# Kernel optimization log

Measured on AMD Instinct MI355X. Metric: run time of the kernel, lower is better.

The kernel has to match this reference:

```python
import jax, jax.numpy as jnp
import numpy as np

N = 50000      # nodes
E = 800000     # edges (before self-loops)
F_IN = 128     # input node features
H = 5          # attention heads
C = 32         # per-head channels (hidden_channels // 5)
HC = H * C     # 160 = hidden_channels
G = 64         # graphs in batch


def setup_inputs() -> dict:
    key = jax.random.key(0)
    ks = jax.random.split(key, 20)
    p = lambda k, shape: jax.random.normal(k, shape, dtype=jnp.float32) * 0.1
    return {
        "x": jax.random.normal(ks[0], (N, F_IN), dtype=jnp.float32),
        "edge_index": jax.random.randint(ks[1], (2, E), 0, N),
        "edge_attr": jax.random.normal(ks[2], (E, 1), dtype=jnp.float32),
        "batch": jnp.sort(jax.random.randint(ks[3], (N,), 0, G)),
        # conv1 params (GATConv: lin, lin_edge, att_src, att_dst, att_edge, bias)
        "w1": p(ks[4], (F_IN, HC)), "we1": p(ks[5], (1, HC)),
        "as1": p(ks[6], (H, C)), "ad1": p(ks[7], (H, C)), "ae1": p(ks[8], (H, C)),
        "b1": jnp.zeros((HC,), jnp.float32),
        # conv2 params
        "w2": p(ks[9], (HC, HC)), "we2": p(ks[10], (1, HC)),
        "as2": p(ks[11], (H, C)), "ad2": p(ks[12], (H, C)), "ae2": p(ks[13], (H, C)),
        "b2": jnp.zeros((HC,), jnp.float32),
        # LayerNorms + merge MLP
        "ln1_g": jnp.ones((HC,), jnp.float32), "ln1_b": jnp.zeros((HC,), jnp.float32),
        "ln2_g": jnp.ones((HC,), jnp.float32), "ln2_b": jnp.zeros((HC,), jnp.float32),
        "mw": p(ks[14], (HC, HC)), "mb": jnp.zeros((HC,), jnp.float32),
    }


def _layernorm(x, g, b, eps=1e-5):
    m = x.mean(-1, keepdims=True)
    v = ((x - m) ** 2).mean(-1, keepdims=True)
    return (x - m) / jnp.sqrt(v + eps) * g + b


def _gat_layer(x, edge_index, edge_attr, w, we, a_s, a_d, a_e, b):
    """PyG GATConv with edge_dim, add_self_loops=True, fill_value='mean'."""
    src, dst = edge_index[0], edge_index[1]
    # self-loop edge_attr = mean of incoming edge attrs (scatter-mean onto dst)
    cnt = jax.ops.segment_sum(jnp.ones((E,), x.dtype), dst, num_segments=N)
    ea_mean = jax.ops.segment_sum(edge_attr, dst, num_segments=N) / jnp.maximum(cnt, 1.0)[:, None]
    loop = jnp.arange(N)
    src_f = jnp.concatenate([src, loop])
    dst_f = jnp.concatenate([dst, loop])
    ea_f = jnp.concatenate([edge_attr, ea_mean], axis=0)  # [E+N, 1]

    h = (x @ w).reshape(N, H, C)                           # [N,H,C]
    al_src = jnp.einsum('nhc,hc->nh', h, a_s)              # [N,H]
    al_dst = jnp.einsum('nhc,hc->nh', h, a_d)
    eh = (ea_f @ we).reshape(-1, H, C)                     # [E+N,H,C]
    al_e = jnp.einsum('ehc,hc->eh', eh, a_e)

    alpha = jax.nn.leaky_relu(al_src[src_f] + al_dst[dst_f] + al_e, 0.2)  # [E+N,H]
    amax = jax.ops.segment_max(alpha, dst_f, num_segments=N)
    ex = jnp.exp(alpha - amax[dst_f])
    den = jax.ops.segment_sum(ex, dst_f, num_segments=N)
    alpha = ex / den[dst_f]                                # segment softmax over dst

    out = jax.ops.segment_sum(h[src_f] * alpha[..., None], dst_f, num_segments=N)
    return out.reshape(N, HC) + b, alpha


def reference(x, edge_index, edge_attr, batch,
              w1, we1, as1, ad1, ae1, b1,
              w2, we2, as2, ad2, ae2, b2,
              ln1_g, ln1_b, ln2_g, ln2_b, mw, mb):
    x1, a1 = _gat_layer(x, edge_index, edge_attr, w1, we1, as1, ad1, ae1, b1)
    x1 = jax.nn.leaky_relu(x1, 0.01)
    x1 = _layernorm(x1, ln1_g, ln1_b)          # dropout = identity in eval
    x2, a2 = _gat_layer(x1, edge_index, edge_attr, w2, we2, as2, ad2, ae2, b2)
    x2 = jax.nn.leaky_relu(x2, 0.01)
    x2 = _layernorm(x2, ln2_g, ln2_b)
    x3 = jax.nn.leaky_relu(x2 @ mw + mb, 0.01)
    gcnt = jax.ops.segment_sum(jnp.ones((N,), x3.dtype), batch, num_segments=G)
    pooled = jax.ops.segment_sum(x3, batch, num_segments=G) / jnp.maximum(gcnt, 1.0)[:, None]
    return x3, pooled, a1, a2
```

## Files before the change

### kernel.cpp

```cpp
#include <hip/hip_runtime.h>
#include <hip/hip_fp16.h>
#include <math.h>

#define NN 50000
#define EE 800000
#define FIN 128
#define NH 5
#define HC 160
#define NG 64
#define CH 128
#define NB 160
#define EPB 5000
#define NW 12500
#define ALS8 8
#define LOG2E 1.4426950408889634f

typedef _Float16 f16x8 __attribute__((ext_vector_type(8)));
typedef _Float16 f16x4 __attribute__((ext_vector_type(4)));
typedef float f32x4 __attribute__((ext_vector_type(4)));

__device__ __forceinline__ float lrelu(float x, float s) { return x >= 0.f ? x : s * x; }

__device__ __forceinline__ float4 h8_to_f4(uint2 u) {
    __half2 a = *reinterpret_cast<__half2*>(&u.x);
    __half2 b = *reinterpret_cast<__half2*>(&u.y);
    float2 fa = __half22float2(a), fb = __half22float2(b);
    return make_float4(fa.x, fa.y, fb.x, fb.y);
}

__global__ void prep_kernel(const int* __restrict__ batch, float* psum, int* gcnt,
                            const float* we1, const float* ae1,
                            const float* we2, const float* ae2, float* s_out) {
    int i = blockIdx.x * 256 + threadIdx.x;
    if (i < NG * HC) psum[i] = 0.f;
    if (i < NG) {
        int lo = 0, hi = NN;
        while (lo < hi) { int m = (lo + hi) >> 1; if (batch[m] < i) lo = m + 1; else hi = m; }
        int s = lo;
        lo = 0; hi = NN;
        int g1 = i + 1;
        while (lo < hi) { int m = (lo + hi) >> 1; if (batch[m] < g1) lo = m + 1; else hi = m; }
        gcnt[i] = lo - s;
    }
    if (i < 10) {
        const float* we = (i < 5) ? we1 : we2;
        const float* ae = (i < 5) ? ae1 : ae2;
        int h = i % 5;
        float s = 0.f;
        for (int c = 0; c < 32; c++) s += we[h * 32 + c] * ae[h * 32 + c];
        s_out[i] = s * LOG2E;
    }
}

__global__ void prepw_kernel(const float* __restrict__ w1, const float* __restrict__ w2,
                             const float* __restrict__ mw,
                             __half* wt1, __half* wt2, __half* wt3) {
    int i = blockIdx.x * 256 + threadIdx.x;
    if (i < 160 * 128) {
        int c = i >> 7, k = i & 127;
        wt1[i] = __float2half(w1[k * HC + c]);
    }
    if (i < 160 * 160) {
        int c = i / 160, k = i - c * 160;
        wt2[i] = __float2half(w2[k * HC + c]);
        wt3[i] = __float2half(mw[k * HC + c]);
    }
}

__global__ __launch_bounds__(256) void hist_kernel(const int* __restrict__ ei,
                                                   unsigned* __restrict__ hist_g) {
    __shared__ unsigned lh[NW];
    int b = blockIdx.x, tid = threadIdx.x;
    for (int w = tid; w < NW; w += 256) lh[w] = 0;
    __syncthreads();
    const int* dstp = ei + EE + b * EPB;
    for (int i = tid; i < EPB; i += 256) {
        int d = dstp[i];
        atomicAdd(&lh[d >> 2], 1u << ((d & 3) * 8));
    }
    __syncthreads();
    unsigned* outp = hist_g + (size_t)b * NW;
    for (int w = tid; w < NW; w += 256) outp[w] = lh[w];
}

__global__ void sscan_kernel(const unsigned* __restrict__ hist_g,
                             unsigned short* __restrict__ base_g, int* __restrict__ deg) {
    int w = blockIdx.x * 256 + threadIdx.x;
    if (w >= NW) return;
    unsigned r0 = 0, r1 = 0, r2 = 0, r3 = 0;
    for (int b = 0; b < NB; b++) {
        unsigned x = hist_g[(size_t)b * NW + w];
        uint2 st;
        st.x = r0 | (r1 << 16);
        st.y = r2 | (r3 << 16);
        *reinterpret_cast<uint2*>(&base_g[(size_t)b * NN + 4 * w]) = st;
        r0 += x & 0xffu; r1 += (x >> 8) & 0xffu; r2 += (x >> 16) & 0xffu; r3 += (x >> 24) & 0xffu;
    }
    uint4 dv; dv.x = r0; dv.y = r1; dv.z = r2; dv.w = r3;
    *reinterpret_cast<uint4*>(&deg[4 * w]) = dv;
}

__global__ void scan1_kernel(const int* __restrict__ deg, int* bsum) {
    __shared__ int ws[4];
    int tid = threadIdx.x, lane = tid & 63, wid = tid >> 6;
    int i = blockIdx.x * 256 + tid;
    int v = (i < NN) ? deg[i] : 0;
    for (int o = 32; o >= 1; o >>= 1) v += __shfl_down(v, o, 64);
    if (lane == 0) ws[wid] = v;
    __syncthreads();
    if (tid == 0) bsum[blockIdx.x] = ws[0] + ws[1] + ws[2] + ws[3];
}

__global__ void scan2_kernel(int* bsum, int* boff) {
    __shared__ int ws[4];
    int tid = threadIdx.x, lane = tid & 63, wid = tid >> 6;
    int v = (tid < 196) ? bsum[tid] : 0;
    int x = v;
    for (int o = 1; o < 64; o <<= 1) {
        int t = __shfl_up(x, o, 64);
        if (lane >= o) x += t;
    }
    if (lane == 63) ws[wid] = x;
    __syncthreads();
    if (tid == 0) {
        int acc = 0;
        for (int w = 0; w < 4; w++) { int t = ws[w]; ws[w] = acc; acc += t; }
    }
    __syncthreads();
    if (tid < 196) boff[tid] = x + ws[wid] - v;
}

__global__ void scan3_kernel(const int* __restrict__ deg, const int* __restrict__ boff,
                             int* off) {
    __shared__ int ws[4];
    int tid = threadIdx.x, lane = tid & 63, wid = tid >> 6;
    int i = blockIdx.x * 256 + tid;
    int v = (i < NN) ? deg[i] : 0;
    int x = v;
    for (int o = 1; o < 64; o <<= 1) {
        int t = __shfl_up(x, o, 64);
        if (lane >= o) x += t;
    }
    if (lane == 63) ws[wid] = x;
    __syncthreads();
    if (tid == 0) {
        int acc = 0;
        for (int w = 0; w < 4; w++) { int t = ws[w]; ws[w] = acc; acc += t; }
    }
    __syncthreads();
    int incl = x + ws[wid] + boff[blockIdx.x];
    if (i < NN) off[i + 1] = incl;
    if (i == 0) off[0] = 0;
}

__global__ __launch_bounds__(256) void scatter_kernel(const int* __restrict__ ei,
                                                      const float* __restrict__ ea,
                                                      const unsigned short* __restrict__ base_g,
                                                      const int* __restrict__ soff,
                                                      uint4* __restrict__ erec) {
    __shared__ unsigned lc[NW];
    int b = blockIdx.x, tid = threadIdx.x;
    for (int w = tid; w < NW; w += 256) lc[w] = 0;
    __syncthreads();
    int e0 = b * EPB;
    const unsigned short* brow = base_g + (size_t)b * NN;
    for (int i = tid; i < EPB; i += 256) {
        int e = e0 + i;
        int d = ei[EE + e];
        int sh = (d & 3) * 8;
        unsigned old = atomicAdd(&lc[d >> 2], 1u << sh);
        int r = (int)((old >> sh) & 0xffu);
        int pos = soff[d] + (int)brow[d] + r;
        uint4 rec;
        rec.x = (unsigned)ei[e];
        rec.y = (unsigned)e;
        rec.z = __float_as_uint(ea[e]);
        rec.w = 0;
        erec[pos] = rec;
    }
}

template <int K, typename AT>
__global__ __launch_bounds__(128, 3) void gemm_kernel(const AT* __restrict__ A,
                                                      const __half* __restrict__ Wt,
                                                      const float* __restrict__ a_s,
                                                      const float* __restrict__ a_d,
                                                      __half* __restrict__ out,
                                                      float* __restrict__ al_s,
                                                      float* __restrict__ al_d) {
    __shared__ __align__(16) _Float16 Alds[32 * 40];
    __shared__ __align__(16) _Float16 Bt[160 * 40];
    __shared__ __align__(16) _Float16 Clds[2 * 32 * 88];
    __shared__ float asld[160], adld[160];
    const int tid = threadIdx.x;
    const int w = tid >> 6, l = tid & 63;
    const int lr = l & 15, lq = l >> 4;
    const int base = blockIdx.x * 32;

    for (int i = tid; i < 160; i += 128) { asld[i] = a_s[i]; adld[i] = a_d[i]; }

    f32x4 acc[2][5];
#pragma unroll
    for (int mt = 0; mt < 2; mt++)
#pragma unroll
        for (int t = 0; t < 5; t++) acc[mt][t] = (f32x4){0.f, 0.f, 0.f, 0.f};

    for (int k0 = 0; k0 < K; k0 += 32) {
        __syncthreads();
        if constexpr (sizeof(AT) == 4) {
            for (int f = tid; f < 256; f += 128) {
                int row = f >> 3, q = f & 7;
                float4 av = make_float4(0.f, 0.f, 0.f, 0.f);
                if (base + row < NN)
                    av = *reinterpret_cast<const float4*>(&A[(size_t)(base + row) * K + k0 + q * 4]);
                f16x4 hv = {(_Float16)av.x, (_Float16)av.y, (_Float16)av.z, (_Float16)av.w};
                *reinterpret_cast<f16x4*>(&Alds[row * 40 + q * 4]) = hv;
            }
        } else {
            int row = tid >> 2, q = tid & 3;
            uint4 v = make_uint4(0, 0, 0, 0);
            if (base + row < NN)
                v = *reinterpret_cast<const uint4*>(&A[(size_t)(base + row) * K + k0 + q * 8]);
            *reinterpret_cast<uint4*>(&Alds[row * 40 + q * 8]) = v;
        }
        for (int f = tid; f < 640; f += 128) {
            int c = f >> 2, q = f & 3;
            uint4 v = *reinterpret_cast<const uint4*>(&Wt[(size_t)c * K + k0 + q * 8]);
            *reinterpret_cast<uint4*>(&Bt[c * 40 + q * 8]) = v;
        }
        __syncthreads();
        const f16x8 a0 = *reinterpret_cast<const f16x8*>(&Alds[lr * 40 + lq * 8]);
        const f16x8 a1 = *reinterpret_cast<const f16x8*>(&Alds[(16 + lr) * 40 + lq * 8]);
#pragma unroll
        for (int t = 0; t < 5; t++) {
            const f16x8 b = *reinterpret_cast<const f16x8*>(
                &Bt[((w * 5 + t) * 16 + lr) * 40 + lq * 8]);
            acc[0][t] = __builtin_amdgcn_mfma_f32_16x16x32_f16(a0, b, acc[0][t], 0, 0, 0);
            acc[1][t] = __builtin_amdgcn_mfma_f32_16x16x32_f16(a1, b, acc[1][t], 0, 0, 0);
        }
    }
    _Float16* Cw = Clds + w * (32 * 88);
#pragma unroll
    for (int mt = 0; mt < 2; mt++)
#pragma unroll
        for (int t = 0; t < 5; t++)
#pragma unroll
            for (int j = 0; j < 4; j++)
                Cw[(mt * 16 + lq * 4 + j) * 88 + t * 16 + lr] = (_Float16)acc[mt][t][j];
    __syncthreads();
    for (int i = l; i < 320; i += 64) {
        int row = i / 10, q = i - row * 10;
        if (base + row < NN) {
            uint4 v = *reinterpret_cast<const uint4*>(&Cw[row * 88 + q * 8]);
            *reinterpret_cast<uint4*>(&out[(size_t)(base + row) * HC + w * 80 + q * 8]) = v;
        }
    }
    for (int f = tid; f < 320; f += 128) {
        int row = f / 10, rem = f - row * 10;
        int h = rem >> 1, sd = rem & 1;
        if (base + row < NN) {
            const float* av = (sd ? adld : asld) + h * 32;
            float s = 0.f;
#pragma unroll
            for (int c = 0; c < 32; c++) {
                int col = h * 32 + c;
                int wv = col >= 80;
                s += (float)Clds[wv * (32 * 88) + row * 88 + (col - 80 * wv)] * av[c];
            }
            s *= LOG2E;
            if (sd) al_d[(size_t)(base + row) * NH + h] = s;
            else    al_s[(size_t)(base + row) * ALS8 + h] = s;
        }
    }
}

__global__ __launch_bounds__(256, 8) void aggregate_kernel(
    const int* __restrict__ soff, const uint4* __restrict__ erec,
    const __half* __restrict__ hfeat, const float* __restrict__ als,
    const float* __restrict__ al_d, const float* __restrict__ s_e,
    const float* __restrict__ bias, const float* __restrict__ g_ln,
    const float* __restrict__ b_ln,
    float* __restrict__ alpha_out, __half* __restrict__ x_out) {
    const int wave = threadIdx.x >> 6;
    const int lane = threadIdx.x & 63;
    const int n = blockIdx.x * 4 + wave;
    __shared__ float w_sh_all[4][CH * NH];
    __shared__ int ioff_all[4][CH];
    float* w_sh = w_sh_all[wave];
    int* ioff_sh = ioff_all[wave];

    const int s0 = soff[n];
    const int deg = soff[n + 1] - s0;
    const int items = deg + 1;

    float adr[NH], ser[NH];
#pragma unroll
    for (int h = 0; h < NH; h++) { adr[h] = al_d[n * NH + h]; ser[h] = s_e[h]; }

    const int c0 = 4 * lane;
    const int hd = lane >> 3;
    float4 acc = make_float4(0.f, 0.f, 0.f, 0.f);

    if (items <= CH) {
        float rw[2][NH];
        float lm[NH];
#pragma unroll
        for (int h = 0; h < NH; h++) lm[h] = -3.0e38f;
        float eas = 0.f;
        int myy[2];
#pragma unroll
        for (int t = 0; t < 2; t++) {
            int i = lane + 64 * t;
            if (i < deg) {
                uint4 rec = erec[s0 + i];
                int src = (int)rec.x;
                float eav = __uint_as_float(rec.z);
                ioff_sh[i] = src * (HC * 2);
                myy[t] = (int)rec.y;
                eas += eav;
                const float* ap = als + (size_t)src * ALS8;
                float4 a4 = *reinterpret_cast<const float4*>(ap);
                float a5 = ap[4];
                float asv[5] = {a4.x, a4.y, a4.z, a4.w, a5};
#pragma unroll
                for (int h = 0; h < NH; h++) {
                    float r = lrelu(asv[h] + adr[h] + eav * ser[h], 0.2f);
                    rw[t][h] = r;
                    lm[h] = fmaxf(lm[h], r);
                }
            }
        }
#pragma unroll
        for (int o = 1; o < 64; o <<= 1) {
#pragma unroll
            for (int h = 0; h < NH; h++) lm[h] = fmaxf(lm[h], __shfl_xor(lm[h], o, 64));
            eas += __shfl_xor(eas, o, 64);
        }
        float emean = eas / fmaxf((float)deg, 1.f);
        float m[NH], rs[NH];
        {
            const float* ap = als + (size_t)n * ALS8;
            float4 a4 = *reinterpret_cast<const float4*>(ap);
            float a5 = ap[4];
            float asv[5] = {a4.x, a4.y, a4.z, a4.w, a5};
#pragma unroll
            for (int h = 0; h < NH; h++) {
                rs[h] = lrelu(asv[h] + adr[h] + emean * ser[h], 0.2f);
                m[h] = fmaxf(lm[h], rs[h]);
            }
        }
        float ls[NH] = {0.f, 0.f, 0.f, 0.f, 0.f};
#pragma unroll
        for (int t = 0; t < 2; t++) {
            int i = lane + 64 * t;
            if (i < deg) {
#pragma unroll
                for (int h = 0; h < NH; h++) {
                    float w = exp2f(rw[t][h] - m[h]);
                    rw[t][h] = w;
                    ls[h] += w;
                }
            } else if (i == deg) {
                ioff_sh[i] = n * (HC * 2);
#pragma unroll
                for (int h = 0; h < NH; h++) {
                    float w = exp2f(rs[h] - m[h]);
                    rw[t][h] = w;
                    ls[h] += w;
                }
            }
        }
#pragma unroll
        for (int o = 1; o < 64; o <<= 1) {
#pragma unroll
            for (int h = 0; h < NH; h++) ls[h] += __shfl_xor(ls[h], o, 64);
        }
        float dinv[NH];
#pragma unroll
        for (int h = 0; h < NH; h++) dinv[h] = 1.f / ls[h];
#pragma unroll
        for (int t = 0; t < 2; t++) {
            int i = lane + 64 * t;
            if (i < items) {
                int opos = (i < deg) ? myy[t] : (EE + n);
#pragma unroll
                for (int h = 0; h < NH; h++) {
                    float w = rw[t][h] * dinv[h];
                    w_sh[i * NH + h] = w;
                    alpha_out[(size_t)opos * NH + h] = w;
                }
            }
        }
        __syncthreads();
        if (lane < 40) {
            const char* hb = (const char*)hfeat + (size_t)(c0 * 2);
            for (int i0 = 0; i0 < items; i0 += 4) {
                float wv[4];
                uint2 hv[4];
#pragma unroll
                for (int j = 0; j < 4; j++) {
                    int i = i0 + j;
                    bool ok = i < items;
                    int ii = ok ? i : 0;
                    wv[j] = ok ? w_sh[ii * NH + hd] : 0.f;
                    hv[j] = *reinterpret_cast<const uint2*>(hb + (size_t)(unsigned)ioff_sh[ii]);
                }
#pragma unroll
                for (int j = 0; j < 4; j++) {
                    __half2 p0 = *reinterpret_cast<__half2*>(&hv[j].x);
                    __half2 p1 = *reinterpret_cast<__half2*>(&hv[j].y);
                    acc.x += wv[j] * __low2float(p0);
                    acc.y += wv[j] * __high2float(p0);
                    acc.z += wv[j] * __low2float(p1);
                    acc.w += wv[j] * __high2float(p1);
                }
            }
        }
    } else {
        float lm[NH];
#pragma unroll
        for (int h = 0; h < NH; h++) lm[h] = -3.0e38f;
        float eas = 0.f;
        for (int i = lane; i < deg; i += 64) {
            uint4 rec = erec[s0 + i];
            int src = (int)rec.x;
            float eav = __uint_as_float(rec.z);
            eas += eav;
            const float* ap = als + (size_t)src * ALS8;
            float4 a4 = *reinterpret_cast<const float4*>(ap);
            float a5 = ap[4];
            float asv[5] = {a4.x, a4.y, a4.z, a4.w, a5};
#pragma unroll
            for (int h = 0; h < NH; h++) {
                float r = lrelu(asv[h] + adr[h] + eav * ser[h], 0.2f);
                lm[h] = fmaxf(lm[h], r);
            }
        }
#pragma unroll
        for (int o = 1; o < 64; o <<= 1) {
#pragma unroll
            for (int h = 0; h < NH; h++) lm[h] = fmaxf(lm[h], __shfl_xor(lm[h], o, 64));
            eas += __shfl_xor(eas, o, 64);
        }
        float emean = eas / fmaxf((float)deg, 1.f);
        float m[NH], rs[NH];
        {
            const float* ap = als + (size_t)n * ALS8;
#pragma unroll
            for (int h = 0; h < NH; h++) {
                rs[h] = lrelu(ap[h] + adr[h] + emean * ser[h], 0.2f);
                m[h] = fmaxf(lm[h], rs[h]);
            }
        }
        float ls[NH] = {0.f, 0.f, 0.f, 0.f, 0.f};
        for (int i = lane; i < items; i += 64) {
            int src; float eav;
            if (i < deg) { uint4 rec = erec[s0 + i]; src = (int)rec.x; eav = __uint_as_float(rec.z); }
            else         { src = n; eav = emean; }
            const float* ap = als + (size_t)src * ALS8;
#pragma unroll
            for (int h = 0; h < NH; h++) {
                float r = lrelu(ap[h] + adr[h] + eav * ser[h], 0.2f);
                ls[h] += exp2f(r - m[h]);
            }
        }
#pragma unroll
        for (int o = 1; o < 64; o <<= 1) {
#pragma unroll
            for (int h = 0; h < NH; h++) ls[h] += __shfl_xor(ls[h], o, 64);
        }
        float dinv[NH];
#pragma unroll
        for (int h = 0; h < NH; h++) dinv[h] = 1.f / ls[h];
        __syncthreads();
        for (int i = lane; i < items; i += 64) {
            int src; float eav; int opos;
            if (i < deg) { uint4 rec = erec[s0 + i]; src = (int)rec.x; eav = __uint_as_float(rec.z); opos = (int)rec.y; }
            else         { src = n; eav = emean; opos = EE + n; }
            const float* ap = als + (size_t)src * ALS8;
#pragma unroll
            for (int h = 0; h < NH; h++) {
                float r = lrelu(ap[h] + adr[h] + eav * ser[h], 0.2f);
                alpha_out[(size_t)opos * NH + h] = exp2f(r - m[h]) * dinv[h];
            }
        }
        if (lane < 40) {
            for (int i = 0; i < items; i++) {
                int src; float eav;
                if (i < deg) { uint4 rec = erec[s0 + i]; src = (int)rec.x; eav = __uint_as_float(rec.z); }
                else         { src = n; eav = emean; }
                float r = lrelu(als[(size_t)src * ALS8 + hd] + adr[hd] + eav * ser[hd], 0.2f);
                float w = exp2f(r - m[hd]) * dinv[hd];
                uint2 hv = *reinterpret_cast<const uint2*>(
                    &hfeat[(size_t)src * HC + c0]);
                float4 hf = h8_to_f4(hv);
                acc.x += w * hf.x; acc.y += w * hf.y;
                acc.z += w * hf.z; acc.w += w * hf.w;
            }
        }
    }

    float4 v = make_float4(0.f, 0.f, 0.f, 0.f);
    float p1 = 0.f, p2 = 0.f;
    if (lane < 40) {
        const float4 b4 = *reinterpret_cast<const float4*>(&bias[c0]);
        v.x = lrelu(acc.x + b4.x, 0.01f);
        v.y = lrelu(acc.y + b4.y, 0.01f);
        v.z = lrelu(acc.z + b4.z, 0.01f);
        v.w = lrelu(acc.w + b4.w, 0.01f);
        p1 = v.x + v.y + v.z + v.w;
        p2 = v.x * v.x + v.y * v.y + v.z * v.z + v.w * v.w;
    }
#pragma unroll
    for (int o = 1; o < 64; o <<= 1) {
        p1 += __shfl_xor(p1, o, 64);
        p2 += __shfl_xor(p2, o, 64);
    }
    float mean = p1 * (1.f / (float)HC);
    float var = p2 * (1.f / (float)HC) - mean * mean;
    float rstd = rsqrtf(var + 1e-5f);
    if (lane < 40) {
        const float4 g4 = *reinterpret_cast<const float4*>(&g_ln[c0]);
        const float4 bb = *reinterpret_cast<const float4*>(&b_ln[c0]);
        float ox = (v.x - mean) * rstd * g4.x + bb.x;
        float oy = (v.y - mean) * rstd * g4.y + bb.y;
        float oz = (v.z - mean) * rstd * g4.z + bb.z;
        float ow = (v.w - mean) * rstd * g4.w + bb.w;
        __half2 h01 = __floats2half2_rn(ox, oy);
        __half2 h23 = __floats2half2_rn(oz, ow);
        uint2 st;
        st.x = *reinterpret_cast<unsigned*>(&h01);
        st.y = *reinterpret_cast<unsigned*>(&h23);
        *reinterpret_cast<uint2*>(&x_out[(size_t)n * HC + c0]) = st;
    }
}

__global__ __launch_bounds__(128, 3) void gemm3_kernel(const __half* __restrict__ A,
                                                       const __half* __restrict__ Wt,
                                                       const float* __restrict__ bias,
                                                       const int* __restrict__ batch,
                                                       float* __restrict__ x3,
                                                       float* __restrict__ psum) {
    __shared__ __align__(16) _Float16 Alds[32 * 40];
    __shared__ __align__(16) _Float16 Bt[160 * 40];
    __shared__ int bt[32];
    const int tid = threadIdx.x;
    const int w = tid >> 6, l = tid & 63;
    const int lr = l & 15, lq = l >> 4;
    const int base = blockIdx.x * 32;

    if (tid < 32) bt[tid] = batch[(base + tid < NN) ? (base + tid) : (NN - 1)];

    f32x4 acc[2][5];
#pragma unroll
    for (int mt = 0; mt < 2; mt++)
#pragma unroll
        for (int t = 0; t < 5; t++) acc[mt][t] = (f32x4){0.f, 0.f, 0.f, 0.f};

    for (int k0 = 0; k0 < HC; k0 += 32) {
        __syncthreads();
        {
            int row = tid >> 2, q = tid & 3;
            uint4 v = make_uint4(0, 0, 0, 0);
            if (base + row < NN)
                v = *reinterpret_cast<const uint4*>(&A[(size_t)(base + row) * HC + k0 + q * 8]);
            *reinterpret_cast<uint4*>(&Alds[row * 40 + q * 8]) = v;
        }
        for (int f = tid; f < 640; f += 128) {
            int c = f >> 2, q = f & 3;
            uint4 v = *reinterpret_cast<const uint4*>(&Wt[(size_t)c * HC + k0 + q * 8]);
            *reinterpret_cast<uint4*>(&Bt[c * 40 + q * 8]) = v;
        }
        __syncthreads();
        const f16x8 a0 = *reinterpret_cast<const f16x8*>(&Alds[lr * 40 + lq * 8]);
        const f16x8 a1 = *reinterpret_cast<const f16x8*>(&Alds[(16 + lr) * 40 + lq * 8]);
#pragma unroll
        for (int t = 0; t < 5; t++) {
            const f16x8 b = *reinterpret_cast<const f16x8*>(
                &Bt[((w * 5 + t) * 16 + lr) * 40 + lq * 8]);
            acc[0][t] = __builtin_amdgcn_mfma_f32_16x16x32_f16(a0, b, acc[0][t], 0, 0, 0);
            acc[1][t] = __builtin_amdgcn_mfma_f32_16x16x32_f16(a1, b, acc[1][t], 0, 0, 0);
        }
    }
#pragma unroll
    for (int t = 0; t < 5; t++) {
        int col = w * 80 + t * 16 + lr;
        float bj = bias[col];
        float run = 0.f;
        int g = bt[lq * 4];
#pragma unroll
        for (int mt = 0; mt < 2; mt++)
#pragma unroll
            for (int j = 0; j < 4; j++) {
                int row = mt * 16 + lq * 4 + j;
                bool ok = base + row < NN;
                float vv = lrelu(acc[mt][t][j] + bj, 0.01f);
                if (ok) x3[(size_t)(base + row) * HC + col] = vv;
                int gb = bt[row];
                if (gb != g) { atomicAdd(&psum[g * HC + col], run); run = 0.f; g = gb; }
                if (ok) run += vv;
            }
        atomicAdd(&psum[g * HC + col], run);
    }
}

__global__ void pooldiv_kernel(const float* __restrict__ psum, const int* __restrict__ gcnt,
                               float* pooled_out) {
    int i = blockIdx.x * 256 + threadIdx.x;
    if (i < NG * HC) pooled_out[i] = psum[i] / fmaxf((float)gcnt[i / HC], 1.f);
}

extern "C" void kernel_launch(void* const* d_in, const int* in_sizes, int n_in,
                              void* d_out, int out_size, void* d_ws, size_t ws_size,
                              hipStream_t stream) {
    const float* x    = (const float*)d_in[0];
    const int*   ei   = (const int*)d_in[1];
    const float* ea   = (const float*)d_in[2];
    const int*   batch= (const int*)d_in[3];
    const float* w1   = (const float*)d_in[4];
    const float* we1  = (const float*)d_in[5];
    const float* as1  = (const float*)d_in[6];
    const float* ad1  = (const float*)d_in[7];
    const float* ae1  = (const float*)d_in[8];
    const float* b1   = (const float*)d_in[9];
    const float* w2   = (const float*)d_in[10];
    const float* we2  = (const float*)d_in[11];
    const float* as2  = (const float*)d_in[12];
    const float* ad2  = (const float*)d_in[13];
    const float* ae2  = (const float*)d_in[14];
    const float* b2   = (const float*)d_in[15];
    const float* ln1g = (const float*)d_in[16];
    const float* ln1b = (const float*)d_in[17];
    const float* ln2g = (const float*)d_in[18];
    const float* ln2b = (const float*)d_in[19];
    const float* mw   = (const float*)d_in[20];
    const float* mb   = (const float*)d_in[21];

    float* out = (float*)d_out;
    float* pooled_out = out + (size_t)NN * HC;
    float* a1 = pooled_out + NG * HC;
    float* a2 = a1 + (size_t)(EE + NN) * NH;

    char* wp = (char*)d_ws;
    auto alloc = [&](size_t bytes) {
        void* p = (void*)wp;
        wp += (bytes + 255) & ~(size_t)255;
        return p;
    };
    char* region = (char*)alloc(32 * 1024 * 1024);
    __half* hbuf = (__half*)region;
    __half* x12h = (__half*)(region + 16 * 1024 * 1024);
    unsigned*       hist_g = (unsigned*)region;
    unsigned short* base_g = (unsigned short*)(region + 8 * 1024 * 1024);
    uint4* erec  = (uint4*)alloc((size_t)EE * 16);
    float* als   = (float*)alloc((size_t)NN * ALS8 * 4);
    float* ald   = (float*)alloc((size_t)NN * NH * 4);
    int*   deg   = (int*)alloc((size_t)NN * 4);
    int*   soff  = (int*)alloc((size_t)(NN + 1) * 4);
    float* sbuf  = (float*)alloc(64);
    float* psum  = (float*)alloc((size_t)NG * HC * 4);
    int*   gcnt  = (int*)alloc((size_t)NG * 4);
    int*   bsum  = (int*)alloc(256 * 4);
    int*   boff  = (int*)alloc(256 * 4);
    __half* wt1  = (__half*)alloc((size_t)160 * 128 * 2);
    __half* wt2  = (__half*)alloc((size_t)160 * 160 * 2);
    __half* wt3  = (__half*)alloc((size_t)160 * 160 * 2);

    prep_kernel<<<40, 256, 0, stream>>>(batch, psum, gcnt, we1, ae1, we2, ae2, sbuf);
    prepw_kernel<<<100, 256, 0, stream>>>(w1, w2, mw, wt1, wt2, wt3);
    hist_kernel<<<NB, 256, 0, stream>>>(ei, hist_g);
    sscan_kernel<<<49, 256, 0, stream>>>(hist_g, base_g, deg);
    scan1_kernel<<<196, 256, 0, stream>>>(deg, bsum);
    scan2_kernel<<<1, 256, 0, stream>>>(bsum, boff);
    scan3_kernel<<<196, 256, 0, stream>>>(deg, boff, soff);
    scatter_kernel<<<NB, 256, 0, stream>>>(ei, ea, base_g, soff, erec);

    const int GB = (NN + 31) / 32;

    gemm_kernel<128, float><<<GB, 128, 0, stream>>>(x, wt1, as1, ad1, hbuf, als, ald);
    aggregate_kernel<<<12500, 256, 0, stream>>>(soff, erec, hbuf, als, ald,
                                                sbuf, b1, ln1g, ln1b, a1, x12h);

    gemm_kernel<160, __half><<<GB, 128, 0, stream>>>(x12h, wt2, as2, ad2, hbuf, als, ald);
    aggregate_kernel<<<12500, 256, 0, stream>>>(soff, erec, hbuf, als, ald,
                                                sbuf + 5, b2, ln2g, ln2b, a2, x12h);

    gemm3_kernel<<<GB, 128, 0, stream>>>(x12h, wt3, mb, batch, out, psum);
    pooldiv_kernel<<<40, 256, 0, stream>>>(psum, gcnt, pooled_out);
}
```

Before: 447.3 us.

## Use 16-lane groups per node in aggregation with degree-sorted node order

The aggregate kernel now gives each node a 16-lane group instead of a full 64-lane wave, so 16 nodes share a block and each lane covers 10 feature channels instead of leaving 24 of 64 lanes idle. A degree histogram and counting sort, built into the existing sscan and scan kernels, produce a permutation that processes nodes in descending degree order to balance work among groups in the same wave. The cost is extra preprocessing, more registers per lane (occupancy hint lowered from 8 to 6), and a small-degree fast path capped at 32 items, with the general path falling back to per-edge recomputation.

```diff
diff --git a/kernel.cpp b/kernel.cpp
--- a/kernel.cpp
+++ b/kernel.cpp
@@ -8,7 +8,7 @@
 #define NH 5
 #define HC 160
 #define NG 64
-#define CH 128
+#define CH2 32
 #define NB 160
 #define EPB 5000
 #define NW 12500
@@ -30,9 +30,11 @@
 
 __global__ void prep_kernel(const int* __restrict__ batch, float* psum, int* gcnt,
                             const float* we1, const float* ae1,
-                            const float* we2, const float* ae2, float* s_out) {
+                            const float* we2, const float* ae2, float* s_out,
+                            int* dbin) {
     int i = blockIdx.x * 256 + threadIdx.x;
     if (i < NG * HC) psum[i] = 0.f;
+    if (i < 256) dbin[i] = 0;
     if (i < NG) {
         int lo = 0, hi = NN;
         while (lo < hi) { int m = (lo + hi) >> 1; if (batch[m] < i) lo = m + 1; else hi = m; }
@@ -84,20 +86,32 @@
 }
 
 __global__ void sscan_kernel(const unsigned* __restrict__ hist_g,
-                             unsigned short* __restrict__ base_g, int* __restrict__ deg) {
-    int w = blockIdx.x * 256 + threadIdx.x;
-    if (w >= NW) return;
-    unsigned r0 = 0, r1 = 0, r2 = 0, r3 = 0;
-    for (int b = 0; b < NB; b++) {
-        unsigned x = hist_g[(size_t)b * NW + w];
-        uint2 st;
-        st.x = r0 | (r1 << 16);
-        st.y = r2 | (r3 << 16);
-        *reinterpret_cast<uint2*>(&base_g[(size_t)b * NN + 4 * w]) = st;
-        r0 += x & 0xffu; r1 += (x >> 8) & 0xffu; r2 += (x >> 16) & 0xffu; r3 += (x >> 24) & 0xffu;
-    }
-    uint4 dv; dv.x = r0; dv.y = r1; dv.z = r2; dv.w = r3;
-    *reinterpret_cast<uint4*>(&deg[4 * w]) = dv;
+                             unsigned short* __restrict__ base_g, int* __restrict__ deg,
+                             int* __restrict__ dbin) {
+    __shared__ int lbin[256];
+    int tid = threadIdx.x;
+    int w = blockIdx.x * 256 + tid;
+    lbin[tid] = 0;
+    __syncthreads();
+    if (w < NW) {
+        unsigned r0 = 0, r1 = 0, r2 = 0, r3 = 0;
+        for (int b = 0; b < NB; b++) {
+            unsigned x = hist_g[(size_t)b * NW + w];
+            uint2 st;
+            st.x = r0 | (r1 << 16);
+            st.y = r2 | (r3 << 16);
+            *reinterpret_cast<uint2*>(&base_g[(size_t)b * NN + 4 * w]) = st;
+            r0 += x & 0xffu; r1 += (x >> 8) & 0xffu; r2 += (x >> 16) & 0xffu; r3 += (x >> 24) & 0xffu;
+        }
+        uint4 dv; dv.x = r0; dv.y = r1; dv.z = r2; dv.w = r3;
+        *reinterpret_cast<uint4*>(&deg[4 * w]) = dv;
+        atomicAdd(&lbin[255 - (int)(r0 > 255u ? 255u : r0)], 1);
+        atomicAdd(&lbin[255 - (int)(r1 > 255u ? 255u : r1)], 1);
+        atomicAdd(&lbin[255 - (int)(r2 > 255u ? 255u : r2)], 1);
+        atomicAdd(&lbin[255 - (int)(r3 > 255u ? 255u : r3)], 1);
+    }
+    __syncthreads();
+    if (lbin[tid]) atomicAdd(&dbin[tid], lbin[tid]);
 }
 
 __global__ void scan1_kernel(const int* __restrict__ deg, int* bsum) {
@@ -111,7 +125,8 @@
     if (tid == 0) bsum[blockIdx.x] = ws[0] + ws[1] + ws[2] + ws[3];
 }
 
-__global__ void scan2_kernel(int* bsum, int* boff) {
+__global__ void scan2_kernel(int* bsum, int* boff, const int* __restrict__ dbin,
+                             int* __restrict__ dpos) {
     __shared__ int ws[4];
     int tid = threadIdx.x, lane = tid & 63, wid = tid >> 6;
     int v = (tid < 196) ? bsum[tid] : 0;
@@ -128,14 +143,32 @@
     }
     __syncthreads();
     if (tid < 196) boff[tid] = x + ws[wid] - v;
+    __syncthreads();
+    int bv = dbin[tid];
+    int bx = bv;
+    for (int o = 1; o < 64; o <<= 1) {
+        int t = __shfl_up(bx, o, 64);
+        if (lane >= o) bx += t;
+    }
+    if (lane == 63) ws[wid] = bx;
+    __syncthreads();
+    if (tid == 0) {
+        int acc = 0;
+        for (int w = 0; w < 4; w++) { int t = ws[w]; ws[w] = acc; acc += t; }
+    }
+    __syncthreads();
+    dpos[tid] = bx + ws[wid] - bv;
 }
 
 __global__ void scan3_kernel(const int* __restrict__ deg, const int* __restrict__ boff,
-                             int* off) {
+                             int* off, int* __restrict__ dpos, int* __restrict__ perm) {
     __shared__ int ws[4];
+    __shared__ int lbin[256];
+    __shared__ int lbase[256];
     int tid = threadIdx.x, lane = tid & 63, wid = tid >> 6;
     int i = blockIdx.x * 256 + tid;
     int v = (i < NN) ? deg[i] : 0;
+    lbin[tid] = 0;
     int x = v;
     for (int o = 1; o < 64; o <<= 1) {
         int t = __shfl_up(x, o, 64);
@@ -149,8 +182,17 @@
     }
     __syncthreads();
     int incl = x + ws[wid] + boff[blockIdx.x];
-    if (i < NN) off[i + 1] = incl;
+    int bin = 255 - (v > 255 ? 255 : v);
+    int rank = 0;
+    if (i < NN) {
+        off[i + 1] = incl;
+        rank = atomicAdd(&lbin[bin], 1);
+    }
     if (i == 0) off[0] = 0;
+    __syncthreads();
+    if (lbin[tid] > 0) lbase[tid] = atomicAdd(&dpos[tid], lbin[tid]);
+    __syncthreads();
+    if (i < NN) perm[lbase[bin] + rank] = i;
 }
 
 __global__ __launch_bounds__(256) void scatter_kernel(const int* __restrict__ ei,
@@ -274,20 +316,22 @@
     }
 }
 
-__global__ __launch_bounds__(256, 8) void aggregate_kernel(
+__global__ __launch_bounds__(256, 6) void aggregate_kernel(
+    const int* __restrict__ perm,
     const int* __restrict__ soff, const uint4* __restrict__ erec,
     const __half* __restrict__ hfeat, const float* __restrict__ als,
     const float* __restrict__ al_d, const float* __restrict__ s_e,
     const float* __restrict__ bias, const float* __restrict__ g_ln,
     const float* __restrict__ b_ln,
     float* __restrict__ alpha_out, __half* __restrict__ x_out) {
-    const int wave = threadIdx.x >> 6;
-    const int lane = threadIdx.x & 63;
-    const int n = blockIdx.x * 4 + wave;
-    __shared__ float w_sh_all[4][CH * NH];
-    __shared__ int ioff_all[4][CH];
-    float* w_sh = w_sh_all[wave];
-    int* ioff_sh = ioff_all[wave];
+    const int tid = threadIdx.x;
+    const int grp = tid >> 4;
+    const int sl = tid & 15;
+    const int n = perm[blockIdx.x * 16 + grp];
+    __shared__ float w_sh_all[16][CH2 * NH];
+    __shared__ int ioff_all[16][CH2];
+    float* w_sh = w_sh_all[grp];
+    int* ioff_sh = ioff_all[grp];
 
     const int s0 = soff[n];
     const int deg = soff[n + 1] - s0;
@@ -297,11 +341,13 @@
 #pragma unroll
     for (int h = 0; h < NH; h++) { adr[h] = al_d[n * NH + h]; ser[h] = s_e[h]; }
 
-    const int c0 = 4 * lane;
-    const int hd = lane >> 3;
-    float4 acc = make_float4(0.f, 0.f, 0.f, 0.f);
-
-    if (items <= CH) {
+    const int cA = sl * 4, cB = 64 + sl * 4, cC = 128 + sl * 2;
+    const int hA = sl >> 3, hB = 2 + (sl >> 3);
+    float4 accA = make_float4(0.f, 0.f, 0.f, 0.f);
+    float4 accB = make_float4(0.f, 0.f, 0.f, 0.f);
+    float2 accC = make_float2(0.f, 0.f);
+
+    if (items <= CH2) {
         float rw[2][NH];
         float lm[NH];
 #pragma unroll
@@ -310,28 +356,30 @@
         int myy[2];
 #pragma unroll
         for (int t = 0; t < 2; t++) {
-            int i = lane + 64 * t;
-            if (i < deg) {
-                uint4 rec = erec[s0 + i];
-                int src = (int)rec.x;
-                float eav = __uint_as_float(rec.z);
-                ioff_sh[i] = src * (HC * 2);
-                myy[t] = (int)rec.y;
-                eas += eav;
-                const float* ap = als + (size_t)src * ALS8;
-                float4 a4 = *reinterpret_cast<const float4*>(ap);
-                float a5 = ap[4];
-                float asv[5] = {a4.x, a4.y, a4.z, a4.w, a5};
-#pragma unroll
-                for (int h = 0; h < NH; h++) {
-                    float r = lrelu(asv[h] + adr[h] + eav * ser[h], 0.2f);
-                    rw[t][h] = r;
-                    lm[h] = fmaxf(lm[h], r);
+            if (deg > 16 * t) {
+                int i = sl + 16 * t;
+                if (i < deg) {
+                    uint4 rec = erec[s0 + i];
+                    int src = (int)rec.x;
+                    float eav = __uint_as_float(rec.z);
+                    ioff_sh[i] = src * (HC * 2);
+                    myy[t] = (int)rec.y;
+                    eas += eav;
+                    const float* ap = als + (size_t)src * ALS8;
+                    float4 a4 = *reinterpret_cast<const float4*>(ap);
+                    float a5 = ap[4];
+                    float asv[5] = {a4.x, a4.y, a4.z, a4.w, a5};
+#pragma unroll
+                    for (int h = 0; h < NH; h++) {
+                        float r = lrelu(asv[h] + adr[h] + eav * ser[h], 0.2f);
+                        rw[t][h] = r;
+                        lm[h] = fmaxf(lm[h], r);
+                    }
                 }
             }
         }
 #pragma unroll
-        for (int o = 1; o < 64; o <<= 1) {
+        for (int o = 1; o < 16; o <<= 1) {
 #pragma unroll
             for (int h = 0; h < NH; h++) lm[h] = fmaxf(lm[h], __shfl_xor(lm[h], o, 64));
             eas += __shfl_xor(eas, o, 64);
@@ -352,68 +400,78 @@
         float ls[NH] = {0.f, 0.f, 0.f, 0.f, 0.f};
 #pragma unroll
         for (int t = 0; t < 2; t++) {
-            int i = lane + 64 * t;
-            if (i < deg) {
-#pragma unroll
-                for (int h = 0; h < NH; h++) {
-                    float w = exp2f(rw[t][h] - m[h]);
-                    rw[t][h] = w;
-                    ls[h] += w;
+            if (items > 16 * t) {
+                int i = sl + 16 * t;
+                if (i < deg) {
+#pragma unroll
+                    for (int h = 0; h < NH; h++) {
+                        float w = exp2f(rw[t][h] - m[h]);
+                        rw[t][h] = w;
+                        ls[h] += w;
+                    }
+                } else if (i == deg) {
+                    ioff_sh[i] = n * (HC * 2);
+#pragma unroll
+                    for (int h = 0; h < NH; h++) {
+                        float w = exp2f(rs[h] - m[h]);
+                        rw[t][h] = w;
+                        ls[h] += w;
+                    }
                 }
-            } else if (i == deg) {
-                ioff_sh[i] = n * (HC * 2);
-#pragma unroll
-                for (int h = 0; h < NH; h++) {
-                    float w = exp2f(rs[h] - m[h]);
-                    rw[t][h] = w;
-                    ls[h] += w;
+            }
+        }
+#pragma unroll
+        for (int o = 1; o < 16; o <<= 1) {
+#pragma unroll
+            for (int h = 0; h < NH; h++) ls[h] += __shfl_xor(ls[h], o, 64);
+        }
+        float dinv[NH];
+#pragma unroll
+        for (int h = 0; h < NH; h++) dinv[h] = 1.f / ls[h];
+#pragma unroll
+        for (int t = 0; t < 2; t++) {
+            if (items > 16 * t) {
+                int i = sl + 16 * t;
+                if (i < items) {
+                    int opos = (i < deg) ? myy[t] : (EE + n);
+#pragma unroll
+                    for (int h = 0; h < NH; h++) {
+                        float w = rw[t][h] * dinv[h];
+                        w_sh[i * NH + h] = w;
+                        alpha_out[(size_t)opos * NH + h] = w;
+                    }
                 }
             }
         }
-#pragma unroll
-        for (int o = 1; o < 64; o <<= 1) {
-#pragma unroll
-            for (int h = 0; h < NH; h++) ls[h] += __shfl_xor(ls[h], o, 64);
-        }
-        float dinv[NH];
-#pragma unroll
-        for (int h = 0; h < NH; h++) dinv[h] = 1.f / ls[h];
-#pragma unroll
-        for (int t = 0; t < 2; t++) {
-            int i = lane + 64 * t;
-            if (i < items) {
-                int opos = (i < deg) ? myy[t] : (EE + n);
-#pragma unroll
-                for (int h = 0; h < NH; h++) {
-                    float w = rw[t][h] * dinv[h];
-                    w_sh[i * NH + h] = w;
-                    alpha_out[(size_t)opos * NH + h] = w;
-                }
-            }
-        }
-        __syncthreads();
-        if (lane < 40) {
-            const char* hb = (const char*)hfeat + (size_t)(c0 * 2);
-            for (int i0 = 0; i0 < items; i0 += 4) {
-                float wv[4];
-                uint2 hv[4];
-#pragma unroll
-                for (int j = 0; j < 4; j++) {
-                    int i = i0 + j;
-                    bool ok = i < items;
-                    int ii = ok ? i : 0;
-                    wv[j] = ok ? w_sh[ii * NH + hd] : 0.f;
-                    hv[j] = *reinterpret_cast<const uint2*>(hb + (size_t)(unsigned)ioff_sh[ii]);
-                }
-#pragma unroll
-                for (int j = 0; j < 4; j++) {
-                    __half2 p0 = *reinterpret_cast<__half2*>(&hv[j].x);
-                    __half2 p1 = *reinterpret_cast<__half2*>(&hv[j].y);
-                    acc.x += wv[j] * __low2float(p0);
-                    acc.y += wv[j] * __high2float(p0);
-                    acc.z += wv[j] * __low2float(p1);
-                    acc.w += wv[j] * __high2float(p1);
-                }
+        const char* hb = (const char*)hfeat;
+        for (int i0 = 0; i0 < items; i0 += 4) {
+            float wA[4], wB[4], wC[4];
+            uint2 vA[4], vB[4];
+            unsigned vC[4];
+#pragma unroll
+            for (int j = 0; j < 4; j++) {
+                int i = i0 + j;
+                bool ok = i < items;
+                int ii = ok ? i : 0;
+                const char* rp = hb + (size_t)(unsigned)ioff_sh[ii];
+                wA[j] = ok ? w_sh[ii * NH + hA] : 0.f;
+                wB[j] = ok ? w_sh[ii * NH + hB] : 0.f;
+                wC[j] = ok ? w_sh[ii * NH + 4] : 0.f;
+                vA[j] = *reinterpret_cast<const uint2*>(rp + cA * 2);
+                vB[j] = *reinterpret_cast<const uint2*>(rp + cB * 2);
+                vC[j] = *reinterpret_cast<const unsigned*>(rp + cC * 2);
+            }
+#pragma unroll
+            for (int j = 0; j < 4; j++) {
+                float4 fA = h8_to_f4(vA[j]);
+                accA.x += wA[j] * fA.x; accA.y += wA[j] * fA.y;
+                accA.z += wA[j] * fA.z; accA.w += wA[j] * fA.w;
+                float4 fB = h8_to_f4(vB[j]);
+                accB.x += wB[j] * fB.x; accB.y += wB[j] * fB.y;
+                accB.z += wB[j] * fB.z; accB.w += wB[j] * fB.w;
+                __half2 pC = *reinterpret_cast<__half2*>(&vC[j]);
+                accC.x += wC[j] * __low2float(pC);
+                accC.y += wC[j] * __high2float(pC);
             }
         }
     } else {
@@ -421,7 +479,7 @@
 #pragma unroll
         for (int h = 0; h < NH; h++) lm[h] = -3.0e38f;
         float eas = 0.f;
-        for (int i = lane; i < deg; i += 64) {
+        for (int i = sl; i < deg; i += 16) {
             uint4 rec = erec[s0 + i];
             int src = (int)rec.x;
             float eav = __uint_as_float(rec.z);
@@ -437,7 +495,7 @@
             }
         }
 #pragma unroll
-        for (int o = 1; o < 64; o <<= 1) {
+        for (int o = 1; o < 16; o <<= 1) {
 #pragma unroll
             for (int h = 0; h < NH; h++) lm[h] = fmaxf(lm[h], __shfl_xor(lm[h], o, 64));
             eas += __shfl_xor(eas, o, 64);
@@ -453,7 +511,7 @@
             }
         }
         float ls[NH] = {0.f, 0.f, 0.f, 0.f, 0.f};
-        for (int i = lane; i < items; i += 64) {
+        for (int i = sl; i < items; i += 16) {
             int src; float eav;
             if (i < deg) { uint4 rec = erec[s0 + i]; src = (int)rec.x; eav = __uint_as_float(rec.z); }
             else         { src = n; eav = emean; }
@@ -465,15 +523,14 @@
             }
         }
 #pragma unroll
-        for (int o = 1; o < 64; o <<= 1) {
+        for (int o = 1; o < 16; o <<= 1) {
 #pragma unroll
             for (int h = 0; h < NH; h++) ls[h] += __shfl_xor(ls[h], o, 64);
         }
         float dinv[NH];
 #pragma unroll
         for (int h = 0; h < NH; h++) dinv[h] = 1.f / ls[h];
-        __syncthreads();
-        for (int i = lane; i < items; i += 64) {
+        for (int i = sl; i < items; i += 16) {
             int src; float eav; int opos;
             if (i < deg) { uint4 rec = erec[s0 + i]; src = (int)rec.x; eav = __uint_as_float(rec.z); opos = (int)rec.y; }
             else         { src = n; eav = emean; opos = EE + n; }
@@ -484,54 +541,86 @@
                 alpha_out[(size_t)opos * NH + h] = exp2f(r - m[h]) * dinv[h];
             }
         }
-        if (lane < 40) {
-            for (int i = 0; i < items; i++) {
-                int src; float eav;
-                if (i < deg) { uint4 rec = erec[s0 + i]; src = (int)rec.x; eav = __uint_as_float(rec.z); }
-                else         { src = n; eav = emean; }
-                float r = lrelu(als[(size_t)src * ALS8 + hd] + adr[hd] + eav * ser[hd], 0.2f);
-                float w = exp2f(r - m[hd]) * dinv[hd];
-                uint2 hv = *reinterpret_cast<const uint2*>(
-                    &hfeat[(size_t)src * HC + c0]);
-                float4 hf = h8_to_f4(hv);
-                acc.x += w * hf.x; acc.y += w * hf.y;
-                acc.z += w * hf.z; acc.w += w * hf.w;
-            }
-        }
-    }
-
-    float4 v = make_float4(0.f, 0.f, 0.f, 0.f);
-    float p1 = 0.f, p2 = 0.f;
-    if (lane < 40) {
-        const float4 b4 = *reinterpret_cast<const float4*>(&bias[c0]);
-        v.x = lrelu(acc.x + b4.x, 0.01f);
-        v.y = lrelu(acc.y + b4.y, 0.01f);
-        v.z = lrelu(acc.z + b4.z, 0.01f);
-        v.w = lrelu(acc.w + b4.w, 0.01f);
-        p1 = v.x + v.y + v.z + v.w;
-        p2 = v.x * v.x + v.y * v.y + v.z * v.z + v.w * v.w;
-    }
-#pragma unroll
-    for (int o = 1; o < 64; o <<= 1) {
+        for (int i = 0; i < items; i++) {
+            int src; float eav;
+            if (i < deg) { uint4 rec = erec[s0 + i]; src = (int)rec.x; eav = __uint_as_float(rec.z); }
+            else         { src = n; eav = emean; }
+            const float* ap = als + (size_t)src * ALS8;
+            float wAv = exp2f(lrelu(ap[hA] + adr[hA] + eav * ser[hA], 0.2f) - m[hA]) * dinv[hA];
+            float wBv = exp2f(lrelu(ap[hB] + adr[hB] + eav * ser[hB], 0.2f) - m[hB]) * dinv[hB];
+            float wCv = exp2f(lrelu(ap[4] + adr[4] + eav * ser[4], 0.2f) - m[4]) * dinv[4];
+            const char* rp = (const char*)hfeat + (size_t)src * (HC * 2);
+            uint2 vA = *reinterpret_cast<const uint2*>(rp + cA * 2);
+            uint2 vB = *reinterpret_cast<const uint2*>(rp + cB * 2);
+            unsigned vC = *reinterpret_cast<const unsigned*>(rp + cC * 2);
+            float4 fA = h8_to_f4(vA);
+            accA.x += wAv * fA.x; accA.y += wAv * fA.y;
+            accA.z += wAv * fA.z; accA.w += wAv * fA.w;
+            float4 fB = h8_to_f4(vB);
+            accB.x += wBv * fB.x; accB.y += wBv * fB.y;
+            accB.z += wBv * fB.z; accB.w += wBv * fB.w;
+            __half2 pC = *reinterpret_cast<__half2*>(&vC);
+            accC.x += wCv * __low2float(pC);
+            accC.y += wCv * __high2float(pC);
+        }
+    }
+
+    const float4 bA = *reinterpret_cast<const float4*>(&bias[cA]);
+    const float4 bB = *reinterpret_cast<const float4*>(&bias[cB]);
+    const float2 bC = *reinterpret_cast<const float2*>(&bias[cC]);
+    float v0 = lrelu(accA.x + bA.x, 0.01f);
+    float v1 = lrelu(accA.y + bA.y, 0.01f);
+    float v2 = lrelu(accA.z + bA.z, 0.01f);
+    float v3 = lrelu(accA.w + bA.w, 0.01f);
+    float v4 = lrelu(accB.x + bB.x, 0.01f);
+    float v5 = lrelu(accB.y + bB.y, 0.01f);
+    float v6 = lrelu(accB.z + bB.z, 0.01f);
+    float v7 = lrelu(accB.w + bB.w, 0.01f);
+    float v8 = lrelu(accC.x + bC.x, 0.01f);
+    float v9 = lrelu(accC.y + bC.y, 0.01f);
+    float p1 = v0 + v1 + v2 + v3 + v4 + v5 + v6 + v7 + v8 + v9;
+    float p2 = v0 * v0 + v1 * v1 + v2 * v2 + v3 * v3 + v4 * v4 +
+               v5 * v5 + v6 * v6 + v7 * v7 + v8 * v8 + v9 * v9;
+#pragma unroll
+    for (int o = 1; o < 16; o <<= 1) {
         p1 += __shfl_xor(p1, o, 64);
         p2 += __shfl_xor(p2, o, 64);
     }
     float mean = p1 * (1.f / (float)HC);
     float var = p2 * (1.f / (float)HC) - mean * mean;
     float rstd = rsqrtf(var + 1e-5f);
-    if (lane < 40) {
-        const float4 g4 = *reinterpret_cast<const float4*>(&g_ln[c0]);
-        const float4 bb = *reinterpret_cast<const float4*>(&b_ln[c0]);
-        float ox = (v.x - mean) * rstd * g4.x + bb.x;
-        float oy = (v.y - mean) * rstd * g4.y + bb.y;
-        float oz = (v.z - mean) * rstd * g4.z + bb.z;
-        float ow = (v.w - mean) * rstd * g4.w + bb.w;
-        __half2 h01 = __floats2half2_rn(ox, oy);
-        __half2 h23 = __floats2half2_rn(oz, ow);
-        uint2 st;
-        st.x = *reinterpret_cast<unsigned*>(&h01);
-        st.y = *reinterpret_cast<unsigned*>(&h23);
-        *reinterpret_cast<uint2*>(&x_out[(size_t)n * HC + c0]) = st;
+    const float4 gA = *reinterpret_cast<const float4*>(&g_ln[cA]);
+    const float4 gB = *reinterpret_cast<const float4*>(&g_ln[cB]);
+    const float2 gC = *reinterpret_cast<const float2*>(&g_ln[cC]);
+    const float4 tA = *reinterpret_cast<const float4*>(&b_ln[cA]);
+    const float4 tB = *reinterpret_cast<const float4*>(&b_ln[cB]);
+    const float2 tC = *reinterpret_cast<const float2*>(&b_ln[cC]);
+    float o0 = (v0 - mean) * rstd * gA.x + tA.x;
+    float o1 = (v1 - mean) * rstd * gA.y + tA.y;
+    float o2 = (v2 - mean) * rstd * gA.z + tA.z;
+    float o3 = (v3 - mean) * rstd * gA.w + tA.w;
+    float o4 = (v4 - mean) * rstd * gB.x + tB.x;
+    float o5 = (v5 - mean) * rstd * gB.y + tB.y;
+    float o6 = (v6 - mean) * rstd * gB.z + tB.z;
+    float o7 = (v7 - mean) * rstd * gB.w + tB.w;
+    float o8 = (v8 - mean) * rstd * gC.x + tC.x;
+    float o9 = (v9 - mean) * rstd * gC.y + tC.y;
+    {
+        __half2 hA01 = __floats2half2_rn(o0, o1);
+        __half2 hA23 = __floats2half2_rn(o2, o3);
+        uint2 stA;
+        stA.x = *reinterpret_cast<unsigned*>(&hA01);
+        stA.y = *reinterpret_cast<unsigned*>(&hA23);
+        *reinterpret_cast<uint2*>(&x_out[(size_t)n * HC + cA]) = stA;
+        __half2 hB01 = __floats2half2_rn(o4, o5);
+        __half2 hB23 = __floats2half2_rn(o6, o7);
+        uint2 stB;
+        stB.x = *reinterpret_cast<unsigned*>(&hB01);
+        stB.y = *reinterpret_cast<unsigned*>(&hB23);
+        *reinterpret_cast<uint2*>(&x_out[(size_t)n * HC + cB]) = stB;
+        __half2 hC = __floats2half2_rn(o8, o9);
+        *reinterpret_cast<unsigned*>(&x_out[(size_t)n * HC + cC]) =
+            *reinterpret_cast<unsigned*>(&hC);
     }
 }
 
@@ -662,28 +751,31 @@
     int*   gcnt  = (int*)alloc((size_t)NG * 4);
     int*   bsum  = (int*)alloc(256 * 4);
     int*   boff  = (int*)alloc(256 * 4);
+    int*   dbin  = (int*)alloc(256 * 4);
+    int*   dpos  = (int*)alloc(256 * 4);
+    int*   perm  = (int*)alloc((size_t)NN * 4);
     __half* wt1  = (__half*)alloc((size_t)160 * 128 * 2);
     __half* wt2  = (__half*)alloc((size_t)160 * 160 * 2);
     __half* wt3  = (__half*)alloc((size_t)160 * 160 * 2);
 
-    prep_kernel<<<40, 256, 0, stream>>>(batch, psum, gcnt, we1, ae1, we2, ae2, sbuf);
+    prep_kernel<<<40, 256, 0, stream>>>(batch, psum, gcnt, we1, ae1, we2, ae2, sbuf, dbin);
     prepw_kernel<<<100, 256, 0, stream>>>(w1, w2, mw, wt1, wt2, wt3);
     hist_kernel<<<NB, 256, 0, stream>>>(ei, hist_g);
-    sscan_kernel<<<49, 256, 0, stream>>>(hist_g, base_g, deg);
+    sscan_kernel<<<49, 256, 0, stream>>>(hist_g, base_g, deg, dbin);
     scan1_kernel<<<196, 256, 0, stream>>>(deg, bsum);
-    scan2_kernel<<<1, 256, 0, stream>>>(bsum, boff);
-    scan3_kernel<<<196, 256, 0, stream>>>(deg, boff, soff);
+    scan2_kernel<<<1, 256, 0, stream>>>(bsum, boff, dbin, dpos);
+    scan3_kernel<<<196, 256, 0, stream>>>(deg, boff, soff, dpos, perm);
     scatter_kernel<<<NB, 256, 0, stream>>>(ei, ea, base_g, soff, erec);
 
     const int GB = (NN + 31) / 32;
 
     gemm_kernel<128, float><<<GB, 128, 0, stream>>>(x, wt1, as1, ad1, hbuf, als, ald);
-    aggregate_kernel<<<12500, 256, 0, stream>>>(soff, erec, hbuf, als, ald,
-                                                sbuf, b1, ln1g, ln1b, a1, x12h);
+    aggregate_kernel<<<3125, 256, 0, stream>>>(perm, soff, erec, hbuf, als, ald,
+                                               sbuf, b1, ln1g, ln1b, a1, x12h);
 
     gemm_kernel<160, __half><<<GB, 128, 0, stream>>>(x12h, wt2, as2, ad2, hbuf, als, ald);
-    aggregate_kernel<<<12500, 256, 0, stream>>>(soff, erec, hbuf, als, ald,
-                                                sbuf + 5, b2, ln2g, ln2b, a2, x12h);
+    aggregate_kernel<<<3125, 256, 0, stream>>>(perm, soff, erec, hbuf, als, ald,
+                                               sbuf + 5, b2, ln2g, ln2b, a2, x12h);
 
     gemm3_kernel<<<GB, 128, 0, stream>>>(x12h, wt3, mb, batch, out, psum);
     pooldiv_kernel<<<40, 256, 0, stream>>>(psum, gcnt, pooled_out);
```

Measured after the change: 447.9 us. No clear change (+0.1%).
